# Kernel optimization log

Measured on AMD Instinct MI355X. Metric: run time of the kernel, lower is better.

Reference implementation:

```python
import jax, jax.numpy as jnp
import numpy as np

RADIUS, HMIN, HMAX, NSAMPLE = 0.05, -0.02, 0.04, 32
EPS = 1e-5


def setup_inputs() -> dict:
    key = jax.random.key(0)
    ks = jax.random.split(key, 6)
    B, N, C, OUT = 4, 2048, 256, 256
    seed_xyz_graspable = jax.random.uniform(ks[0], (B, N, 3), jnp.float32) * 0.2
    seed_features_graspable = jax.random.normal(ks[1], (B, C, N), jnp.float32)
    vp_rot = jax.random.normal(ks[2], (B, N, 3, 3), jnp.float32)
    W1 = jax.random.normal(ks[3], (OUT, 3 + C), jnp.float32) * 0.02
    W2 = jax.random.normal(ks[4], (OUT, OUT), jnp.float32) * 0.02
    return {
        "seed_xyz_graspable": seed_xyz_graspable,
        "seed_features_graspable": seed_features_graspable,
        "vp_rot": vp_rot,
        "W1": W1, "gamma1": jnp.ones((OUT,), jnp.float32), "beta1": jnp.zeros((OUT,), jnp.float32),
        "W2": W2, "gamma2": jnp.ones((OUT,), jnp.float32), "beta2": jnp.zeros((OUT,), jnp.float32),
    }


def _cylinder_query(xyz, rot):
    # xyz: (B,N,3), rot: (B,N,3,3); new_xyz == xyz.
    B, N, _ = xyz.shape
    d = xyz[:, None, :, :] - xyz[:, :, None, :]                  # (B,P,N,3) offsets to each candidate
    r = jnp.einsum('bpij,bpnj->bpni', rot, d)                    # rotate into cylinder frame (rot @ d)
    mask = (r[..., 1] ** 2 + r[..., 2] ** 2 < RADIUS ** 2) & (r[..., 0] > HMIN) & (r[..., 0] < HMAX)
    order = jnp.arange(N, dtype=jnp.int32)
    keys = jnp.where(mask, order, order + N)                     # in-cylinder points sort first, stable order
    _, idx = jax.lax.top_k(-keys, NSAMPLE)                       # first NSAMPLE indices satisfying the query
    valid = jnp.take_along_axis(mask, idx, axis=-1)
    first = idx[..., :1]
    any_valid = valid[..., :1]
    idx = jnp.where(valid, idx, jnp.where(any_valid, first, 0))  # pad with first hit like the CUDA kernel
    return idx                                                   # (B,P,NSAMPLE) int32


def _group(xyz, features, rot, idx):
    gxyz = jax.vmap(lambda a, i: a[i])(xyz, idx)                 # (B,P,S,3)
    gxyz = (gxyz - xyz[:, :, None, :]) / RADIUS                  # center on query + normalize_xyz
    gxyz = jnp.einsum('bpsj,bpjk->bpsk', gxyz, rot)              # rotate_xyz: grouped_xyz @ rot
    gfeat = jax.vmap(lambda f, i: f[:, i])(features, idx)        # (B,C,P,S)
    return jnp.concatenate([gxyz.transpose(0, 3, 1, 2), gfeat], axis=1)  # (B,3+C,P,S)


def _conv_bn_relu(x, W, gamma, beta):
    y = jnp.einsum('oc,bcps->bops', W, x)                        # 1x1 conv, no bias (bn=True)
    mu = y.mean(axis=(0, 2, 3), keepdims=True)
    var = y.var(axis=(0, 2, 3), keepdims=True)
    y = (y - mu) * jax.lax.rsqrt(var + EPS)
    y = y * gamma[None, :, None, None] + beta[None, :, None, None]
    return jax.nn.relu(y)


def reference(seed_xyz_graspable, seed_features_graspable, vp_rot, W1, gamma1, beta1, W2, gamma2, beta2):
    idx = _cylinder_query(seed_xyz_graspable, vp_rot)
    g = _group(seed_xyz_graspable, seed_features_graspable, vp_rot, idx)
    h = _conv_bn_relu(g, W1, gamma1, beta1)
    h = _conv_bn_relu(h, W2, gamma2, beta2)
    return h.max(axis=3)                                         # maxpool over nsample -> (B,OUT,P)
```

## Files before the change

kernel.cpp:

```cpp
#include <hip/hip_runtime.h>

typedef unsigned short u16;
typedef unsigned int u32;
typedef __attribute__((ext_vector_type(8))) short bf16x8;
typedef __attribute__((ext_vector_type(4))) float f32x4;

#define NPTS 2048
#define CFEAT 256
#define NS 32
#define MTOT 262144
#define NBLK 4096
#define NROW 8192
#define INV_N (1.0f/262144.0f)

__device__ __forceinline__ float bf2f(u16 u) {
    union { u32 i; float f; } v; v.i = ((u32)u) << 16; return v.f;
}
__device__ __forceinline__ u16 f2bf(float f) {
    union { float f; u32 i; } v; v.f = f;
    u32 i = v.i;
    return (u16)((i + 0x7fffu + ((i >> 16) & 1u)) >> 16);
}

__device__ __forceinline__ void gload16(const void* g, void* l) {
    __builtin_amdgcn_global_load_lds((const __attribute__((address_space(1))) void*)g,
                                     (__attribute__((address_space(3))) void*)l, 16, 0, 0);
}

__global__ __launch_bounds__(256) void prep_k(const float* __restrict__ W1, const float* __restrict__ W2,
                                              u16* __restrict__ Wp1, u16* __restrict__ Wp2) {
    int o = blockIdx.x, t = threadIdx.x;
    Wp1[o * 288 + t] = f2bf(W1[o * 259 + 3 + t]);
    if (t < 32) Wp1[o * 288 + 256 + t] = (t < 3) ? f2bf(W1[o * 259 + t]) : (u16)0;
    Wp2[o * 256 + t] = f2bf(W2[o * 256 + t]);
}

__global__ __launch_bounds__(256) void query_k(const float* __restrict__ xyz, const float* __restrict__ rot,
                                               int* __restrict__ idx) {
    int pid = blockIdx.x * 4 + (threadIdx.x >> 6);
    int lane = threadIdx.x & 63;
    int b = pid >> 11, p = pid & 2047;
    const float* xb = xyz + (size_t)b * NPTS * 3;
    float px = xb[p * 3 + 0], py = xb[p * 3 + 1], pz = xb[p * 3 + 2];
    const float* rp = rot + (size_t)pid * 9;
    float r00 = rp[0], r01 = rp[1], r02 = rp[2];
    float r10 = rp[3], r11 = rp[4], r12 = rp[5];
    float r20 = rp[6], r21 = rp[7], r22 = rp[8];
    int cnt = 0, first = 0;
    for (int n0 = 0; n0 < NPTS && cnt < NS; n0 += 64) {
        int n = n0 + lane;
        float dx = __fsub_rn(xb[n * 3 + 0], px);
        float dy = __fsub_rn(xb[n * 3 + 1], py);
        float dz = __fsub_rn(xb[n * 3 + 2], pz);
        float a0 = __fadd_rn(__fadd_rn(__fmul_rn(r00, dx), __fmul_rn(r01, dy)), __fmul_rn(r02, dz));
        float a1 = __fadd_rn(__fadd_rn(__fmul_rn(r10, dx), __fmul_rn(r11, dy)), __fmul_rn(r12, dz));
        float a2 = __fadd_rn(__fadd_rn(__fmul_rn(r20, dx), __fmul_rn(r21, dy)), __fmul_rn(r22, dz));
        float t2 = __fadd_rn(__fmul_rn(a1, a1), __fmul_rn(a2, a2));
        bool valid = (t2 < 0.0025f) && (a0 > -0.02f) && (a0 < 0.04f);
        unsigned long long bal = __ballot(valid);
        if (cnt == 0 && bal) first = n0 + __builtin_ctzll(bal);
        int rank = __builtin_popcountll(bal & ((1ull << lane) - 1ull));
        int slot = cnt + rank;
        if (valid && slot < NS) idx[(size_t)pid * NS + slot] = n;
        cnt += __builtin_popcountll(bal);
    }
    int filled = cnt < NS ? cnt : NS;
    if (lane >= filled && lane < NS) idx[(size_t)pid * NS + lane] = (cnt > 0) ? first : 0;
}

__global__ __launch_bounds__(256) void featT_k(const float* __restrict__ feat, u16* __restrict__ featT) {
    __shared__ float sm[32 * 33];
    int b = blockIdx.z;
    int n0 = blockIdx.x * 32, c0 = blockIdx.y * 32;
    int t = threadIdx.x, x = t & 31, y = t >> 5;
    #pragma unroll
    for (int rr = 0; rr < 4; rr++) {
        int c = c0 + y + rr * 8;
        sm[(y + rr * 8) * 33 + x] = feat[((size_t)(b * CFEAT + c)) * NPTS + n0 + x];
    }
    __syncthreads();
    #pragma unroll
    for (int rr = 0; rr < 4; rr++) {
        int n = n0 + y + rr * 8;
        featT[((size_t)(b * NPTS + n)) * CFEAT + c0 + x] = f2bf(sm[x * 33 + (y + rr * 8)]);
    }
}

__global__ __launch_bounds__(256) void gxyz_k(const float* __restrict__ xyz, const float* __restrict__ rot,
                                              const int* __restrict__ idx, u16* __restrict__ gxyz) {
    int m = blockIdx.x * 256 + threadIdx.x;
    int pid = m >> 5;
    int b = pid >> 11, p = pid & 2047;
    int i = idx[m];
    const float* xb = xyz + (size_t)b * NPTS * 3;
    float dx = (xb[i * 3 + 0] - xb[p * 3 + 0]) * 20.0f;
    float dy = (xb[i * 3 + 1] - xb[p * 3 + 1]) * 20.0f;
    float dz = (xb[i * 3 + 2] - xb[p * 3 + 2]) * 20.0f;
    const float* rp = rot + (size_t)pid * 9;
    float g0 = dx * rp[0] + dy * rp[3] + dz * rp[6];
    float g1 = dx * rp[1] + dy * rp[4] + dz * rp[7];
    float g2 = dx * rp[2] + dy * rp[5] + dz * rp[8];
    uint2 v;
    v.x = (u32)f2bf(g0) | ((u32)f2bf(g1) << 16);
    v.y = (u32)f2bf(g2);
    *(uint2*)(gxyz + (size_t)m * 4) = v;
}

__global__ __launch_bounds__(256) void hist_k(const int* __restrict__ idx, const u16* __restrict__ gxyz,
                                              float* __restrict__ hpart, float* __restrict__ xst64) {
    __shared__ float hist[8192];
    __shared__ float red[9 * 4];
    const int t = threadIdx.x, lane = t & 63, wave = t >> 6;
    const int g = blockIdx.x;
    const int base = g * 4096;
    for (int i = t; i < 8192; i += 256) hist[i] = 0.f;
    __syncthreads();
    float p[9] = {0.f,0.f,0.f,0.f,0.f,0.f,0.f,0.f,0.f};
    for (int u = 0; u < 16; u++) {
        int m = base + u * 256 + t;
        int r = idx[m];
        uint2 v = *(const uint2*)(gxyz + (size_t)m * 4);
        float x0 = bf2f((u16)(v.x & 0xffff));
        float x1 = bf2f((u16)(v.x >> 16));
        float x2 = bf2f((u16)(v.y & 0xffff));
        atomicAdd(hist + r * 4 + 0, 1.f);
        atomicAdd(hist + r * 4 + 1, x0);
        atomicAdd(hist + r * 4 + 2, x1);
        atomicAdd(hist + r * 4 + 3, x2);
        p[0] += x0; p[1] += x1; p[2] += x2;
        p[3] += x0 * x0; p[4] += x0 * x1; p[5] += x0 * x2;
        p[6] += x1 * x1; p[7] += x1 * x2; p[8] += x2 * x2;
    }
    __syncthreads();
    for (int i = t; i < 8192; i += 256) hpart[(size_t)g * 8192 + i] = hist[i];
    #pragma unroll
    for (int k = 0; k < 9; k++) {
        float s = p[k];
        #pragma unroll
        for (int o = 1; o < 64; o <<= 1) s += __shfl_xor(s, o);
        if (lane == 0) red[k * 4 + wave] = s;
    }
    __syncthreads();
    if (t < 9) xst64[g * 9 + t] = red[t * 4 + 0] + red[t * 4 + 1] + red[t * 4 + 2] + red[t * 4 + 3];
}

__global__ __launch_bounds__(256) void zgemm_k(const u16* __restrict__ featT, const u16* __restrict__ Wp1,
                                               const float* __restrict__ hpart,
                                               float* __restrict__ Sacc, float* __restrict__ Qacc,
                                               float* __restrict__ Xacc) {
    __shared__ __attribute__((aligned(16))) u16 As[64 * 32];
    __shared__ __attribute__((aligned(16))) u16 Bs[256 * 32];
    __shared__ float cxs[64 * 4];
    const int tid = threadIdx.x;
    const int lane = tid & 63, wave = tid >> 6;
    const int quad = lane >> 4, tl = lane & 15;
    const int m0 = blockIdx.x * 64;
    const int srow = tid >> 2, sc16 = tid & 3;
    const int abase = (m0 + srow) * CFEAT + sc16 * 8;

    {
        const int b = m0 >> 11;
        const int rl0 = m0 & 2047;
        int row = tid >> 2, c = tid & 3;
        float s = 0.f;
        #pragma unroll
        for (int sg = 0; sg < 16; sg++)
            s += hpart[(size_t)(b * 16 + sg) * 8192 + (rl0 + row) * 4 + c];
        cxs[tid] = s;
    }

    f32x4 acc[4][4];
    #pragma unroll
    for (int i = 0; i < 4; i++)
        #pragma unroll
        for (int j = 0; j < 4; j++) acc[i][j] = (f32x4){0.f, 0.f, 0.f, 0.f};

    for (int ks = 0; ks < 8; ks++) {
        const int k0 = ks * 32;
        __syncthreads();
        gload16(featT + abase + k0, As + tid * 8);
        #pragma unroll
        for (int q = 0; q < 4; q++)
            gload16(Wp1 + (srow + q * 64) * 288 + k0 + sc16 * 8, Bs + q * 2048 + tid * 8);
        __syncthreads();
        bf16x8 af[4], bv[4];
        #pragma unroll
        for (int i = 0; i < 4; i++) af[i] = *(const bf16x8*)(As + (i * 16 + tl) * 32 + quad * 8);
        #pragma unroll
        for (int j = 0; j < 4; j++) bv[j] = *(const bf16x8*)(Bs + (wave * 64 + j * 16 + tl) * 32 + quad * 8);
        #pragma unroll
        for (int i = 0; i < 4; i++)
            #pragma unroll
            for (int j = 0; j < 4; j++)
                acc[i][j] = __builtin_amdgcn_mfma_f32_16x16x32_bf16(af[i], bv[j], acc[i][j], 0, 0, 0);
    }

    #pragma unroll
    for (int j = 0; j < 4; j++) {
        int col = wave * 64 + j * 16 + tl;
        float wx0 = bf2f(Wp1[col * 288 + 256]);
        float wx1 = bf2f(Wp1[col * 288 + 257]);
        float wx2 = bf2f(Wp1[col * 288 + 258]);
        float S = 0.f, Q = 0.f, X = 0.f;
        #pragma unroll
        for (int i = 0; i < 4; i++)
            #pragma unroll
            for (int rr = 0; rr < 4; rr++) {
                int row = i * 16 + quad * 4 + rr;
                float4 cx = *(const float4*)(cxs + row * 4);
                float z = acc[i][j][rr];
                S += cx.x * z;
                Q += cx.x * z * z;
                X += z * (wx0 * cx.y + wx1 * cx.z + wx2 * cx.w);
            }
        S += __shfl_xor(S, 16); S += __shfl_xor(S, 32);
        Q += __shfl_xor(Q, 16); Q += __shfl_xor(Q, 32);
        X += __shfl_xor(X, 16); X += __shfl_xor(X, 32);
        if (quad == 0) {
            atomicAdd(Sacc + col, S);
            atomicAdd(Qacc + col, Q);
            atomicAdd(Xacc + col, X);
        }
    }
}

__global__ __launch_bounds__(256) void ab1_k(const float* __restrict__ Sacc, const float* __restrict__ Qacc,
                                             const float* __restrict__ Xacc, const float* __restrict__ xst64,
                                             const u16* __restrict__ Wp1,
                                             const float* __restrict__ gamma, const float* __restrict__ beta,
                                             float* __restrict__ ab) {
    int c = threadIdx.x;
    float xs[9] = {0.f,0.f,0.f,0.f,0.f,0.f,0.f,0.f,0.f};
    for (int g = 0; g < 64; g++)
        #pragma unroll
        for (int k = 0; k < 9; k++) xs[k] += xst64[g * 9 + k];
    float wx0 = bf2f(Wp1[c * 288 + 256]);
    float wx1 = bf2f(Wp1[c * 288 + 257]);
    float wx2 = bf2f(Wp1[c * 288 + 258]);
    float S = Sacc[c] + wx0 * xs[0] + wx1 * xs[1] + wx2 * xs[2];
    float qxx = wx0 * wx0 * xs[3] + wx1 * wx1 * xs[6] + wx2 * wx2 * xs[8]
              + 2.f * (wx0 * wx1 * xs[4] + wx0 * wx2 * xs[5] + wx1 * wx2 * xs[7]);
    float Q = Qacc[c] + 2.f * Xacc[c] + qxx;
    float mu = S * INV_N;
    float var = Q * INV_N - mu * mu;
    float a = gamma[c] * rsqrtf(var + 1e-5f);
    ab[c] = a;
    ab[256 + c] = beta[c] - mu * a;
}

template <int FULL>
__global__ __launch_bounds__(256, 3) void fused_k(
    const u16* __restrict__ featT, const u16* __restrict__ gxyz, const int* __restrict__ idx,
    const u16* __restrict__ Wp1, const u16* __restrict__ Wp2, const float* __restrict__ ab1,
    float* __restrict__ psum, float* __restrict__ psq,
    float* __restrict__ ymax, float* __restrict__ ymin)
{
    __shared__ __attribute__((aligned(16))) u16 As[64 * 32];
    __shared__ __attribute__((aligned(16))) u16 Bs[256 * 32];
    __shared__ __attribute__((aligned(16))) u16 y1s[FULL ? 64 * 136 : 16];
    __shared__ int rowbase_s[64];

    const int tid = threadIdx.x;
    const int lane = tid & 63, wave = tid >> 6;
    const int quad = lane >> 4, tl = lane & 15;
    const int bx = blockIdx.x;
    const int m0 = bx * 64;

    if (tid < 64) {
        int m = m0 + tid;
        int gi = idx[m];
        int b = m >> 16;
        rowbase_s[tid] = (b * NPTS + gi) * CFEAT;
    }
    __syncthreads();
    const int srow = tid >> 2, sc16 = tid & 3;
    const int abase = rowbase_s[srow] + sc16 * 8;

    f32x4 acc[4][4];
    #pragma unroll
    for (int i = 0; i < 4; i++)
        #pragma unroll
        for (int j = 0; j < 4; j++) acc[i][j] = (f32x4){0.f, 0.f, 0.f, 0.f};

    auto mfma_tile = [&](f32x4 (&ac)[4][4], const u16* a_lds, int a_stride) {
        bf16x8 af[4], bv[4];
        #pragma unroll
        for (int i = 0; i < 4; i++) af[i] = *(const bf16x8*)(a_lds + (i * 16 + tl) * a_stride + quad * 8);
        #pragma unroll
        for (int j = 0; j < 4; j++) bv[j] = *(const bf16x8*)(Bs + (j * 64 + wave * 16 + tl) * 32 + quad * 8);
        #pragma unroll
        for (int i = 0; i < 4; i++)
            #pragma unroll
            for (int j = 0; j < 4; j++)
                ac[i][j] = __builtin_amdgcn_mfma_f32_16x16x32_bf16(af[i], bv[j], ac[i][j], 0, 0, 0);
    };

    for (int ks = 0; ks < 8; ks++) {
        const int k0 = ks * 32;
        __syncthreads();
        gload16(featT + abase + k0, As + tid * 8);
        #pragma unroll
        for (int q = 0; q < 4; q++)
            gload16(Wp1 + (srow + q * 64) * 288 + k0 + sc16 * 8, Bs + q * 2048 + tid * 8);
        __syncthreads();
        mfma_tile(acc, As, 32);
    }
    {
        __syncthreads();
        uint4 va = make_uint4(0, 0, 0, 0);
        if (sc16 == 0) {
            uint2 g2 = *(const uint2*)(gxyz + (size_t)(m0 + srow) * 4);
            va.x = g2.x; va.y = g2.y;
        }
        *(uint4*)(As + srow * 32 + sc16 * 8) = va;
        #pragma unroll
        for (int q = 0; q < 4; q++)
            gload16(Wp1 + (srow + q * 64) * 288 + 256 + sc16 * 8, Bs + q * 2048 + tid * 8);
        __syncthreads();
        mfma_tile(acc, As, 32);
    }

    if (!FULL) {
        #pragma unroll
        for (int j = 0; j < 4; j++) {
            float s = 0.f, q2 = 0.f;
            #pragma unroll
            for (int i = 0; i < 4; i++) {
                s += acc[i][j][0] + acc[i][j][1] + acc[i][j][2] + acc[i][j][3];
                q2 += acc[i][j][0]*acc[i][j][0] + acc[i][j][1]*acc[i][j][1]
                    + acc[i][j][2]*acc[i][j][2] + acc[i][j][3]*acc[i][j][3];
            }
            s += __shfl_xor(s, 16); s += __shfl_xor(s, 32);
            q2 += __shfl_xor(q2, 16); q2 += __shfl_xor(q2, 32);
            if (quad == 0) {
                int col = j * 64 + wave * 16 + tl;
                psum[(size_t)bx * 256 + col] = s;
                psq[(size_t)bx * 256 + col] = q2;
            }
        }
        return;
    }

    #pragma unroll
    for (int j = 0; j < 2; j++) {
        int col = j * 64 + wave * 16 + tl;
        float a = ab1[col], bb = ab1[256 + col];
        #pragma unroll
        for (int i = 0; i < 4; i++)
            #pragma unroll
            for (int r = 0; r < 4; r++) {
                float v = fmaxf(fmaf(acc[i][j][r], a, bb), 0.f);
                y1s[(i * 16 + quad * 4 + r) * 136 + col] = f2bf(v);
            }
    }

    f32x4 acc2[4][4];
    #pragma unroll
    for (int i = 0; i < 4; i++)
        #pragma unroll
        for (int j = 0; j < 4; j++) acc2[i][j] = (f32x4){0.f, 0.f, 0.f, 0.f};
    for (int ks = 0; ks < 8; ks++) {
        if (ks == 4) {
            __syncthreads();
            #pragma unroll
            for (int j = 2; j < 4; j++) {
                int col = j * 64 + wave * 16 + tl;
                int lc = col - 128;
                float a = ab1[col], bb = ab1[256 + col];
                #pragma unroll
                for (int i = 0; i < 4; i++)
                    #pragma unroll
                    for (int r = 0; r < 4; r++) {
                        float v = fmaxf(fmaf(acc[i][j][r], a, bb), 0.f);
                        y1s[(i * 16 + quad * 4 + r) * 136 + lc] = f2bf(v);
                    }
            }
        }
        const int k0 = ks * 32;
        const int kl = k0 & 127;
        __syncthreads();
        #pragma unroll
        for (int q = 0; q < 4; q++)
            gload16(Wp2 + (srow + q * 64) * 256 + k0 + sc16 * 8, Bs + q * 2048 + tid * 8);
        __syncthreads();
        mfma_tile(acc2, y1s + kl, 136);
    }

    #pragma unroll
    for (int j = 0; j < 4; j++) {
        int col = j * 64 + wave * 16 + tl;
        float s = 0.f, q2 = 0.f;
        float mx0 = -3.0e38f, mn0 = 3.0e38f, mx1 = -3.0e38f, mn1 = 3.0e38f;
        #pragma unroll
        for (int i = 0; i < 4; i++)
            #pragma unroll
            for (int r = 0; r < 4; r++) {
                float v = acc2[i][j][r];
                s += v; q2 += v * v;
                if (i < 2) { mx0 = fmaxf(mx0, v); mn0 = fminf(mn0, v); }
                else       { mx1 = fmaxf(mx1, v); mn1 = fminf(mn1, v); }
            }
        s += __shfl_xor(s, 16); s += __shfl_xor(s, 32);
        q2 += __shfl_xor(q2, 16); q2 += __shfl_xor(q2, 32);
        mx0 = fmaxf(mx0, __shfl_xor(mx0, 16)); mx0 = fmaxf(mx0, __shfl_xor(mx0, 32));
        mn0 = fminf(mn0, __shfl_xor(mn0, 16)); mn0 = fminf(mn0, __shfl_xor(mn0, 32));
        mx1 = fmaxf(mx1, __shfl_xor(mx1, 16)); mx1 = fmaxf(mx1, __shfl_xor(mx1, 32));
        mn1 = fminf(mn1, __shfl_xor(mn1, 16)); mn1 = fminf(mn1, __shfl_xor(mn1, 32));
        if (quad == 0) {
            psum[(size_t)bx * 256 + col] = s;
            psq[(size_t)bx * 256 + col] = q2;
            size_t p0 = (size_t)(bx * 2) * 256 + col;
            size_t p1 = (size_t)(bx * 2 + 1) * 256 + col;
            ymax[p0] = mx0; ymin[p0] = mn0;
            ymax[p1] = mx1; ymin[p1] = mn1;
        }
    }
}

__global__ __launch_bounds__(256) void reduce1_k(const float* __restrict__ psum, const float* __restrict__ psq,
                                                 float* __restrict__ ps2, float* __restrict__ pq2) {
    int j = blockIdx.x, t = threadIdx.x;
    float s = 0.f, q = 0.f;
    #pragma unroll 4
    for (int kk = 0; kk < 64; kk++) {
        size_t r = (size_t)(j * 64 + kk) * 256 + t;
        s += psum[r]; q += psq[r];
    }
    ps2[j * 256 + t] = s;
    pq2[j * 256 + t] = q;
}

__global__ __launch_bounds__(256) void reduce2_k(const float* __restrict__ ps2, const float* __restrict__ pq2,
                                                 const float* __restrict__ gamma, const float* __restrict__ beta,
                                                 float* __restrict__ ab) {
    int c = threadIdx.x;
    float S = 0.f, Q = 0.f;
    for (int j = 0; j < 64; j++) {
        S += ps2[j * 256 + c];
        Q += pq2[j * 256 + c];
    }
    float mu = S * INV_N;
    float var = Q * INV_N - mu * mu;
    float a = gamma[c] * rsqrtf(var + 1e-5f);
    ab[c] = a;
    ab[256 + c] = beta[c] - mu * a;
}

__global__ __launch_bounds__(256) void final_k(const float* __restrict__ ymax, const float* __restrict__ ymin,
                                               const float* __restrict__ ab, float* __restrict__ out) {
    __shared__ float sm[32 * 33];
    int b = blockIdx.z;
    int n0 = blockIdx.x * 32, o0 = blockIdx.y * 32;
    int t = threadIdx.x, x = t & 31, y = t >> 5;
    #pragma unroll
    for (int rr = 0; rr < 4; rr++) {
        int n = n0 + y + rr * 8;
        int o = o0 + x;
        float a = ab[o], bb = ab[256 + o];
        size_t p = (size_t)(b * NPTS + n) * 256 + o;
        float v = (a >= 0.f) ? ymax[p] : ymin[p];
        sm[(y + rr * 8) * 33 + x] = fmaxf(fmaf(v, a, bb), 0.f);
    }
    __syncthreads();
    #pragma unroll
    for (int rr = 0; rr < 4; rr++)
        out[((size_t)(b * 256 + o0 + y + rr * 8)) * NPTS + n0 + x] = sm[x * 33 + (y + rr * 8)];
}

extern "C" void kernel_launch(void* const* d_in, const int* in_sizes, int n_in,
                              void* d_out, int out_size, void* d_ws, size_t ws_size,
                              hipStream_t stream) {
    const float* xyz    = (const float*)d_in[0];
    const float* feat   = (const float*)d_in[1];
    const float* rot    = (const float*)d_in[2];
    const float* W1     = (const float*)d_in[3];
    const float* gamma1 = (const float*)d_in[4];
    const float* beta1  = (const float*)d_in[5];
    const float* W2     = (const float*)d_in[6];
    const float* gamma2 = (const float*)d_in[7];
    const float* beta2  = (const float*)d_in[8];
    float* out = (float*)d_out;

    char* ws = (char*)d_ws;
    u16*   featT = (u16*)(ws + 0);
    int*   idxp  = (int*)(ws + 4194304);
    u16*   gxyz  = (u16*)(ws + 5242880);
    u16*   Wp1   = (u16*)(ws + 7340032);
    u16*   Wp2   = (u16*)(ws + 7487488);
    float* ab1   = (float*)(ws + 7618560);
    float* ab2   = (float*)(ws + 7620608);
    float* Sacc  = (float*)(ws + 7753728);
    float* Qacc  = (float*)(ws + 7754752);
    float* Xacc  = (float*)(ws + 7755776);
    float* xst64 = (float*)(ws + 7756800);
    float* hpart = (float*)(ws + 7760896);
    float* psum  = (float*)(ws + 9858048);
    float* psq   = (float*)(ws + 14052352);
    float* ymax  = (float*)(ws + 18246656);
    float* ymin  = (float*)(ws + 26635264);
    const size_t NEED = 35023872ull;

    float* r1s = (float*)(ws + 26635264);
    float* r1q = r1s + 16384;
    float* r2s = (float*)(ws + 5242880);
    float* r2q = r2s + 16384;

    prep_k<<<256, 256, 0, stream>>>(W1, W2, Wp1, Wp2);
    query_k<<<2048, 256, 0, stream>>>(xyz, rot, idxp);
    featT_k<<<dim3(64, 8, 4), 256, 0, stream>>>(feat, featT);
    gxyz_k<<<1024, 256, 0, stream>>>(xyz, rot, idxp, gxyz);

    if (ws_size >= NEED) {
        hipMemsetAsync(Sacc, 0, 3 * 1024, stream);
        hist_k<<<64, 256, 0, stream>>>(idxp, gxyz, hpart, xst64);
        zgemm_k<<<NROW / 64, 256, 0, stream>>>(featT, Wp1, hpart, Sacc, Qacc, Xacc);
        ab1_k<<<1, 256, 0, stream>>>(Sacc, Qacc, Xacc, xst64, Wp1, gamma1, beta1, ab1);
        fused_k<1><<<NBLK, 256, 0, stream>>>(featT, gxyz, idxp, Wp1, Wp2, ab1, psum, psq, ymax, ymin);
        reduce1_k<<<64, 256, 0, stream>>>(psum, psq, r2s, r2q);
        reduce2_k<<<1, 256, 0, stream>>>(r2s, r2q, gamma2, beta2, ab2);
    } else {
        fused_k<0><<<NBLK, 256, 0, stream>>>(featT, gxyz, idxp, Wp1, Wp2, ab1, psum, psq, ymax, ymin);
        reduce1_k<<<64, 256, 0, stream>>>(psum, psq, r1s, r1q);
        reduce2_k<<<1, 256, 0, stream>>>(r1s, r1q, gamma1, beta1, ab1);
        fused_k<1><<<NBLK, 256, 0, stream>>>(featT, gxyz, idxp, Wp1, Wp2, ab1, psum, psq, ymax, ymin);
        reduce1_k<<<64, 256, 0, stream>>>(psum, psq, r2s, r2q);
        reduce2_k<<<1, 256, 0, stream>>>(r2s, r2q, gamma2, beta2, ab2);
    }
    final_k<<<dim3(64, 8, 4), 256, 0, stream>>>(ymax, ymin, ab2, out);
}
```

Measured before the change: 267.4 us.

## Fold prep and memset into other kernels, register-prefetch gathered A rows

Weight bf16 packing moves into the first 256 blocks of query_k, and the Sacc zeroing moves into hist_k block 0, removing one kernel launch and one memset. In fused_k, all gathered feature rows plus the xyz slice are loaded into registers up front and then written to LDS each k-step, replacing the per-step global-to-LDS gathers. Occupancy is raised from 3 to 4 blocks per CU through launch bounds, and the second GEMM loop is unrolled. The register prefetch and the higher occupancy target add register pressure, which risks spills. hist_k zeroes Sacc in block 0 while zgemm_k accumulates into it; this is safe only because zgemm_k runs after hist_k on the same stream.

New measurement: 308.9 us. +15.5%, slower.

```diff
diff --git a/kernel.cpp b/kernel.cpp
--- a/kernel.cpp
+++ b/kernel.cpp
@@ -27,16 +27,16 @@
                                      (__attribute__((address_space(3))) void*)l, 16, 0, 0);
 }
 
-__global__ __launch_bounds__(256) void prep_k(const float* __restrict__ W1, const float* __restrict__ W2,
-                                              u16* __restrict__ Wp1, u16* __restrict__ Wp2) {
-    int o = blockIdx.x, t = threadIdx.x;
-    Wp1[o * 288 + t] = f2bf(W1[o * 259 + 3 + t]);
-    if (t < 32) Wp1[o * 288 + 256 + t] = (t < 3) ? f2bf(W1[o * 259 + t]) : (u16)0;
-    Wp2[o * 256 + t] = f2bf(W2[o * 256 + t]);
-}
-
 __global__ __launch_bounds__(256) void query_k(const float* __restrict__ xyz, const float* __restrict__ rot,
-                                               int* __restrict__ idx) {
+                                               int* __restrict__ idx,
+                                               const float* __restrict__ W1, const float* __restrict__ W2,
+                                               u16* __restrict__ Wp1, u16* __restrict__ Wp2) {
+    if (blockIdx.x < 256) {
+        int o = blockIdx.x, t = threadIdx.x;
+        Wp1[o * 288 + t] = f2bf(W1[o * 259 + 3 + t]);
+        if (t < 32) Wp1[o * 288 + 256 + t] = (t < 3) ? f2bf(W1[o * 259 + t]) : (u16)0;
+        Wp2[o * 256 + t] = f2bf(W2[o * 256 + t]);
+    }
     int pid = blockIdx.x * 4 + (threadIdx.x >> 6);
     int lane = threadIdx.x & 63;
     int b = pid >> 11, p = pid & 2047;
@@ -107,12 +107,14 @@
 }
 
 __global__ __launch_bounds__(256) void hist_k(const int* __restrict__ idx, const u16* __restrict__ gxyz,
-                                              float* __restrict__ hpart, float* __restrict__ xst64) {
+                                              float* __restrict__ hpart, float* __restrict__ xst64,
+                                              float* __restrict__ Sacc) {
     __shared__ float hist[8192];
     __shared__ float red[9 * 4];
     const int t = threadIdx.x, lane = t & 63, wave = t >> 6;
     const int g = blockIdx.x;
     const int base = g * 4096;
+    if (g == 0) { Sacc[t] = 0.f; Sacc[t + 256] = 0.f; Sacc[t + 512] = 0.f; }
     for (int i = t; i < 8192; i += 256) hist[i] = 0.f;
     __syncthreads();
     float p[9] = {0.f,0.f,0.f,0.f,0.f,0.f,0.f,0.f,0.f};
@@ -249,7 +251,7 @@
 }
 
 template <int FULL>
-__global__ __launch_bounds__(256, 3) void fused_k(
+__global__ __launch_bounds__(256, 4) void fused_k(
     const u16* __restrict__ featT, const u16* __restrict__ gxyz, const int* __restrict__ idx,
     const u16* __restrict__ Wp1, const u16* __restrict__ Wp2, const float* __restrict__ ab1,
     float* __restrict__ psum, float* __restrict__ psq,
@@ -276,46 +278,44 @@
     const int srow = tid >> 2, sc16 = tid & 3;
     const int abase = rowbase_s[srow] + sc16 * 8;
 
-    f32x4 acc[4][4];
-    #pragma unroll
-    for (int i = 0; i < 4; i++)
-        #pragma unroll
-        for (int j = 0; j < 4; j++) acc[i][j] = (f32x4){0.f, 0.f, 0.f, 0.f};
-
-    auto mfma_tile = [&](f32x4 (&ac)[4][4], const u16* a_lds, int a_stride) {
-        bf16x8 af[4], bv[4];
-        #pragma unroll
-        for (int i = 0; i < 4; i++) af[i] = *(const bf16x8*)(a_lds + (i * 16 + tl) * a_stride + quad * 8);
-        #pragma unroll
-        for (int j = 0; j < 4; j++) bv[j] = *(const bf16x8*)(Bs + (j * 64 + wave * 16 + tl) * 32 + quad * 8);
-        #pragma unroll
-        for (int i = 0; i < 4; i++)
-            #pragma unroll
-            for (int j = 0; j < 4; j++)
-                ac[i][j] = __builtin_amdgcn_mfma_f32_16x16x32_bf16(af[i], bv[j], ac[i][j], 0, 0, 0);
-    };
-
-    for (int ks = 0; ks < 8; ks++) {
-        const int k0 = ks * 32;
-        __syncthreads();
-        gload16(featT + abase + k0, As + tid * 8);
-        #pragma unroll
-        for (int q = 0; q < 4; q++)
-            gload16(Wp1 + (srow + q * 64) * 288 + k0 + sc16 * 8, Bs + q * 2048 + tid * 8);
-        __syncthreads();
-        mfma_tile(acc, As, 32);
-    }
+    uint4 a_pre[9];
+    #pragma unroll
+    for (int t = 0; t < 8; t++) a_pre[t] = *(const uint4*)(featT + abase + t * 32);
     {
-        __syncthreads();
         uint4 va = make_uint4(0, 0, 0, 0);
         if (sc16 == 0) {
             uint2 g2 = *(const uint2*)(gxyz + (size_t)(m0 + srow) * 4);
             va.x = g2.x; va.y = g2.y;
         }
-        *(uint4*)(As + srow * 32 + sc16 * 8) = va;
+        a_pre[8] = va;
+    }
+
+    f32x4 acc[4][4];
+    #pragma unroll
+    for (int i = 0; i < 4; i++)
+        #pragma unroll
+        for (int j = 0; j < 4; j++) acc[i][j] = (f32x4){0.f, 0.f, 0.f, 0.f};
+
+    auto mfma_tile = [&](f32x4 (&ac)[4][4], const u16* a_lds, int a_stride) {
+        bf16x8 af[4], bv[4];
+        #pragma unroll
+        for (int i = 0; i < 4; i++) af[i] = *(const bf16x8*)(a_lds + (i * 16 + tl) * a_stride + quad * 8);
+        #pragma unroll
+        for (int j = 0; j < 4; j++) bv[j] = *(const bf16x8*)(Bs + (j * 64 + wave * 16 + tl) * 32 + quad * 8);
+        #pragma unroll
+        for (int i = 0; i < 4; i++)
+            #pragma unroll
+            for (int j = 0; j < 4; j++)
+                ac[i][j] = __builtin_amdgcn_mfma_f32_16x16x32_bf16(af[i], bv[j], ac[i][j], 0, 0, 0);
+    };
+
+    #pragma unroll
+    for (int t = 0; t < 9; t++) {
+        __syncthreads();
+        *(uint4*)(As + tid * 8) = a_pre[t];
         #pragma unroll
         for (int q = 0; q < 4; q++)
-            gload16(Wp1 + (srow + q * 64) * 288 + 256 + sc16 * 8, Bs + q * 2048 + tid * 8);
+            gload16(Wp1 + (srow + q * 64) * 288 + t * 32 + sc16 * 8, Bs + q * 2048 + tid * 8);
         __syncthreads();
         mfma_tile(acc, As, 32);
     }
@@ -359,6 +359,7 @@
     for (int i = 0; i < 4; i++)
         #pragma unroll
         for (int j = 0; j < 4; j++) acc2[i][j] = (f32x4){0.f, 0.f, 0.f, 0.f};
+    #pragma unroll
     for (int ks = 0; ks < 8; ks++) {
         if (ks == 4) {
             __syncthreads();
@@ -505,14 +506,12 @@
     float* r2s = (float*)(ws + 5242880);
     float* r2q = r2s + 16384;
 
-    prep_k<<<256, 256, 0, stream>>>(W1, W2, Wp1, Wp2);
-    query_k<<<2048, 256, 0, stream>>>(xyz, rot, idxp);
+    query_k<<<2048, 256, 0, stream>>>(xyz, rot, idxp, W1, W2, Wp1, Wp2);
     featT_k<<<dim3(64, 8, 4), 256, 0, stream>>>(feat, featT);
     gxyz_k<<<1024, 256, 0, stream>>>(xyz, rot, idxp, gxyz);
 
     if (ws_size >= NEED) {
-        hipMemsetAsync(Sacc, 0, 3 * 1024, stream);
-        hist_k<<<64, 256, 0, stream>>>(idxp, gxyz, hpart, xst64);
+        hist_k<<<64, 256, 0, stream>>>(idxp, gxyz, hpart, xst64, Sacc);
         zgemm_k<<<NROW / 64, 256, 0, stream>>>(featT, Wp1, hpart, Sacc, Qacc, Xacc);
         ab1_k<<<1, 256, 0, stream>>>(Sacc, Qacc, Xacc, xst64, Wp1, gamma1, beta1, ab1);
         fused_k<1><<<NBLK, 256, 0, stream>>>(featT, gxyz, idxp, Wp1, Wp2, ab1, psum, psq, ymax, ymin);
```
